# Performance work log

Measured on AMD Instinct MI355X. Metric: run time of the kernel, lower is better.

The kernel has to match this reference:

```python
import jax, jax.numpy as jnp
import numpy as np

D = 1024
SCALE = 10.0  # forward does qk.div(1/10) == qk * 10


def setup_inputs() -> dict:
    key = jax.random.key(0)
    ks = jax.random.split(key, 9)
    B, S = 8, 2048
    lim = 1.0 / np.sqrt(D)  # torch Linear default init range
    return {
        "query": jax.random.normal(ks[0], (B, S, D), jnp.float32),
        "key": jax.random.normal(ks[1], (B, S, D), jnp.float32),
        "value": jax.random.normal(ks[2], (B, S, D), jnp.float32),
        "Wq": jax.random.uniform(ks[3], (D, D), jnp.float32, -lim, lim),
        "bq": jax.random.uniform(ks[4], (D,), jnp.float32, -lim, lim),
        "Wk": jax.random.uniform(ks[5], (D, D), jnp.float32, -lim, lim),
        "bk": jax.random.uniform(ks[6], (D,), jnp.float32, -lim, lim),
        "Wv": jax.random.uniform(ks[7], (D, D), jnp.float32, -lim, lim),
        "bv": jax.random.uniform(ks[8], (D,), jnp.float32, -lim, lim),
    }


def reference(query, key, value, Wq, bq, Wk, bk, Wv, bv):
    # torch Linear: x @ W.T + b
    q = jnp.einsum("bsd,ed->bse", query, Wq) + bq
    k = jnp.einsum("bsd,ed->bse", key, Wk) + bk
    v = jnp.einsum("bsd,ed->bse", value, Wv) + bv
    qk = jnp.einsum("bqd,bkd->bqk", q, k)
    scaled_qk = qk * SCALE  # qk.div(1.0 / scale_factor)
    softmax_qk = jax.nn.softmax(scaled_qk, axis=-1)
    # dropout in eval mode == identity (deterministic reference)
    output = jnp.einsum("bqk,bkd->bqd", softmax_qk, v)
    return (output, softmax_qk)
```

## Files before the change

### kernel.cpp

```cpp
#include <hip/hip_runtime.h>

typedef unsigned short u16;
typedef unsigned int u32;
typedef __bf16 bf16x8 __attribute__((ext_vector_type(8)));
typedef float f32x4 __attribute__((ext_vector_type(4)));

__device__ __forceinline__ u16 bf16_rne(float f) {
  u32 u = __float_as_uint(f);
  u += 0x7fffu + ((u >> 16) & 1u);
  return (u16)(u >> 16);
}
__device__ __forceinline__ float bf16_to_f(u16 h) {
  return __uint_as_float(((u32)h) << 16);
}
__device__ __forceinline__ void gload16(const u16* g, u16* l) {
  __builtin_amdgcn_global_load_lds(
      (const __attribute__((address_space(1))) void*)g,
      (__attribute__((address_space(3))) void*)l, 16, 0, 0);
}

__global__ __launch_bounds__(256) void split_kernel(const float* __restrict__ x,
                                                    u16* __restrict__ hi,
                                                    u16* __restrict__ lo, int n8) {
  int i = blockIdx.x * 256 + threadIdx.x;
  if (i >= n8) return;
  float4 a = ((const float4*)x)[2 * i];
  float4 b = ((const float4*)x)[2 * i + 1];
  float v[8] = {a.x, a.y, a.z, a.w, b.x, b.y, b.z, b.w};
  union { u16 u[8]; uint4 q; } H, L;
#pragma unroll
  for (int j = 0; j < 8; ++j) H.u[j] = bf16_rne(v[j]);
  ((uint4*)hi)[i] = H.q;
  if (lo != nullptr) {
#pragma unroll
    for (int j = 0; j < 8; ++j) L.u[j] = bf16_rne(v[j] - bf16_to_f(H.u[j]));
    ((uint4*)lo)[i] = L.q;
  }
}

__global__ __launch_bounds__(256) void transpose_split(const float* __restrict__ in,
                                                       u16* __restrict__ hiT,
                                                       u16* __restrict__ loT) {
  __shared__ float tile[32][33];
  const int t = threadIdx.x;
  const int r0 = blockIdx.y * 32, c0 = blockIdx.x * 32;
  const int x = t & 31, y = t >> 5;
#pragma unroll
  for (int i = 0; i < 4; ++i)
    tile[y + i * 8][x] = in[(size_t)(r0 + y + i * 8) * 1024 + c0 + x];
  __syncthreads();
#pragma unroll
  for (int i = 0; i < 4; ++i) {
    float v = tile[x][y + i * 8];
    u16 h = bf16_rne(v);
    u16 l = bf16_rne(v - bf16_to_f(h));
    size_t o = (size_t)(c0 + y + i * 8) * 1024 + r0 + x;
    hiT[o] = h;
    loT[o] = l;
  }
}

__global__ __launch_bounds__(256) void zero_vec(float* __restrict__ h) {
  h[blockIdx.x * 256 + threadIdx.x] = 0.f;
}

__global__ __launch_bounds__(256) void colvec_kernel(const float* __restrict__ W,
                                                     const float* __restrict__ b,
                                                     float* __restrict__ h) {
  __shared__ float sb[16];
  const int t = threadIdx.x;
  const int e0 = blockIdx.x * 16;
  if (t < 16) sb[t] = b[e0 + t];
  __syncthreads();
  float a0 = 0.f, a1 = 0.f, a2 = 0.f, a3 = 0.f;
#pragma unroll
  for (int i = 0; i < 16; ++i) {
    const float* row = W + (size_t)(e0 + i) * 1024;
    const float be = sb[i];
    a0 += row[t] * be;
    a1 += row[t + 256] * be;
    a2 += row[t + 512] * be;
    a3 += row[t + 768] * be;
  }
  atomicAdd(&h[t], a0);
  atomicAdd(&h[t + 256], a1);
  atomicAdd(&h[t + 512], a2);
  atomicAdd(&h[t + 768], a3);
}

__global__ __launch_bounds__(256) void rowdot_kernel(const float* __restrict__ X,
                                                     const float* __restrict__ h,
                                                     float* __restrict__ w) {
  const int t = threadIdx.x, lane = t & 63, wv = t >> 6;
  const size_t row = (size_t)blockIdx.x * 4 + wv;
  const float4* xr = (const float4*)(X + row * 1024);
  const float4* hr = (const float4*)h;
  float acc = 0.f;
#pragma unroll
  for (int j = 0; j < 4; ++j) {
    float4 a = xr[lane + j * 64];
    float4 b = hr[lane + j * 64];
    acc += a.x * b.x + a.y * b.y + a.z * b.z + a.w * b.w;
  }
#pragma unroll
  for (int o = 32; o > 0; o >>= 1) acc += __shfl_xor(acc, o, 64);
  if (lane == 0) w[row] = acc;
}

template <int NPROD, int EPI>
__global__ __launch_bounds__(256) void gemm_bt(
    const u16* __restrict__ Ah, const u16* __restrict__ Al,
    const u16* __restrict__ Bh, const u16* __restrict__ Bl,
    const float* __restrict__ bias,
    u16* __restrict__ Ch, u16* __restrict__ Cl,
    float* __restrict__ Cf, float scale, int K,
    int lda, int ldb, int ldc,
    long long batchA, long long batchB, long long batchC) {
  __shared__ u16 sAh[4096];
  __shared__ u16 sBh[4096];
  __shared__ u16 sAl[NPROD == 3 ? 4096 : 64];
  __shared__ u16 sBl[NPROD == 3 ? 4096 : 64];

  const int t = threadIdx.x;
  const int w = t >> 6;
  const int lane = t & 63;
  const int m0 = blockIdx.y * 128;
  const int n0 = blockIdx.x * 128;
  const long long z = blockIdx.z;

  Ah += z * batchA;
  Bh += z * batchB;

  const int rS = t >> 2;
  const int cS = (((t & 3) ^ ((t >> 3) & 3))) * 8;
  const u16* pAh = Ah + (size_t)(m0 + rS) * lda + cS;
  const u16* pBh = Bh + (size_t)(n0 + rS) * ldb + cS;
  const u16* pAl = nullptr;
  const u16* pBl = nullptr;
  if constexpr (NPROD == 3) {
    pAl = Al + z * batchA + (size_t)(m0 + rS) * lda + cS;
    pBl = Bl + z * batchB + (size_t)(n0 + rS) * ldb + cS;
  }

  const int wr = (w >> 1) * 64;
  const int wc = (w & 1) * 64;
  const int fr = lane & 15;
  const int cc = lane >> 4;
  const int fk = (cc ^ ((fr >> 1) & 3)) * 8;

  f32x4 acc[4][4];
#pragma unroll
  for (int i = 0; i < 4; ++i)
#pragma unroll
    for (int j = 0; j < 4; ++j) acc[i][j] = (f32x4){0.f, 0.f, 0.f, 0.f};

  for (int k0 = 0; k0 < K; k0 += 32) {
    __syncthreads();
#pragma unroll
    for (int j = 0; j < 2; ++j) {
      gload16(pAh + (size_t)j * 64 * lda + k0, &sAh[j * 2048 + w * 512]);
      gload16(pBh + (size_t)j * 64 * ldb + k0, &sBh[j * 2048 + w * 512]);
      if constexpr (NPROD == 3) {
        gload16(pAl + (size_t)j * 64 * lda + k0, &sAl[j * 2048 + w * 512]);
        gload16(pBl + (size_t)j * 64 * ldb + k0, &sBl[j * 2048 + w * 512]);
      }
    }
    __syncthreads();
    bf16x8 ah[4], bh[4], al[4], bl[4];
#pragma unroll
    for (int i = 0; i < 4; ++i) {
      ah[i] = *(const bf16x8*)&sAh[(wr + i * 16 + fr) * 32 + fk];
      bh[i] = *(const bf16x8*)&sBh[(wc + i * 16 + fr) * 32 + fk];
      if constexpr (NPROD == 3) {
        al[i] = *(const bf16x8*)&sAl[(wr + i * 16 + fr) * 32 + fk];
        bl[i] = *(const bf16x8*)&sBl[(wc + i * 16 + fr) * 32 + fk];
      }
    }
#pragma unroll
    for (int i = 0; i < 4; ++i)
#pragma unroll
      for (int j = 0; j < 4; ++j) {
        acc[i][j] = __builtin_amdgcn_mfma_f32_16x16x32_bf16(ah[i], bh[j], acc[i][j], 0, 0, 0);
        if constexpr (NPROD == 3) {
          acc[i][j] = __builtin_amdgcn_mfma_f32_16x16x32_bf16(ah[i], bl[j], acc[i][j], 0, 0, 0);
          acc[i][j] = __builtin_amdgcn_mfma_f32_16x16x32_bf16(al[i], bh[j], acc[i][j], 0, 0, 0);
        }
      }
  }

  if constexpr (EPI >= 2) Cf += z * batchC;

#pragma unroll
  for (int i = 0; i < 4; ++i) {
    const int row0 = m0 + wr + i * 16 + ((lane >> 4) << 2);
#pragma unroll
    for (int j = 0; j < 4; ++j) {
      const int col = n0 + wc + j * 16 + (lane & 15);
      if constexpr (EPI == 0) {
        const float b = bias ? bias[col] : 0.0f;
#pragma unroll
        for (int r = 0; r < 4; ++r) {
          float c = acc[i][j][r] + b;
          u16 h = bf16_rne(c);
          u16 l = bf16_rne(c - bf16_to_f(h));
          size_t o = (size_t)(row0 + r) * ldc + col;
          Ch[o] = h;
          Cl[o] = l;
        }
      } else if constexpr (EPI == 1) {
        const float b = bias[col];
        ushort4 pk;
        pk.x = bf16_rne(acc[i][j][0] + b);
        pk.y = bf16_rne(acc[i][j][1] + b);
        pk.z = bf16_rne(acc[i][j][2] + b);
        pk.w = bf16_rne(acc[i][j][3] + b);
        const int bb = row0 >> 11;
        const int s = row0 & 2047;
        *(ushort4*)&Ch[(size_t)bb * 2097152 + (size_t)col * 2048 + s] = pk;
      } else if constexpr (EPI == 2) {
#pragma unroll
        for (int r = 0; r < 4; ++r)
          Cf[(size_t)(row0 + r) * ldc + col] = acc[i][j][r] * scale;
      } else {
        const float wv = bias[(size_t)z * 2048 + col];
#pragma unroll
        for (int r = 0; r < 4; ++r)
          Cf[(size_t)(row0 + r) * ldc + col] = (acc[i][j][r] + wv) * scale;
      }
    }
  }
}

template <int NPROD, int EPI>
__global__ __launch_bounds__(512) void gemm256(
    const u16* __restrict__ Ah, const u16* __restrict__ Al,
    const u16* __restrict__ Bh, const u16* __restrict__ Bl,
    const float* __restrict__ bias,
    u16* __restrict__ Ch, u16* __restrict__ Cl,
    float* __restrict__ Cf, float scale, int K,
    int lda, int ldb, int ldc,
    long long batchA, long long batchB, long long batchC) {
  __shared__ u16 sAh[2][8192];
  __shared__ u16 sBh[2][8192];
  __shared__ u16 sAl[NPROD == 3 ? 16384 : 8];
  __shared__ u16 sBl[NPROD == 3 ? 16384 : 8];

  const int t = threadIdx.x;
  const int w = t >> 6;
  const int lane = t & 63;
  const int m0 = blockIdx.y * 256;
  const int n0 = blockIdx.x * 256;
  const long long z = blockIdx.z;

  const int rS = t >> 2;
  const int cS = ((t & 3) ^ ((rS >> 1) & 3)) * 8;
  const u16* pAh = Ah + z * batchA + (size_t)(m0 + rS) * lda + cS;
  const u16* pBh = Bh + z * batchB + (size_t)(n0 + rS) * ldb + cS;
  const u16* pAl = nullptr;
  const u16* pBl = nullptr;
  if constexpr (NPROD == 3) {
    pAl = Al + z * batchA + (size_t)(m0 + rS) * lda + cS;
    pBl = Bl + z * batchB + (size_t)(n0 + rS) * ldb + cS;
  }

  const int wr = (w >> 2) * 128;
  const int wc = (w & 3) * 64;
  const int fr = lane & 15;
  const int fk = (((lane >> 4) ^ ((fr >> 1) & 3)) * 8);

  f32x4 acc[8][4];
#pragma unroll
  for (int i = 0; i < 8; ++i)
#pragma unroll
    for (int j = 0; j < 4; ++j) acc[i][j] = (f32x4){0.f, 0.f, 0.f, 0.f};

  auto SAH = [&](int b, int k0) {
    gload16(pAh + k0, &sAh[b][w * 512]);
    gload16(pAh + (size_t)128 * lda + k0, &sAh[b][4096 + w * 512]);
  };
  auto SBH = [&](int b, int k0) {
    gload16(pBh + k0, &sBh[b][w * 512]);
    gload16(pBh + (size_t)128 * ldb + k0, &sBh[b][4096 + w * 512]);
  };
  auto SAL = [&](int b, int k0) {
    gload16(pAl + k0, &sAl[b * 8192 + w * 512]);
    gload16(pAl + (size_t)128 * lda + k0, &sAl[b * 8192 + 4096 + w * 512]);
  };
  auto SBL = [&](int b, int k0) {
    gload16(pBl + k0, &sBl[b * 8192 + w * 512]);
    gload16(pBl + (size_t)128 * ldb + k0, &sBl[b * 8192 + 4096 + w * 512]);
  };

  SAH(0, 0);
  SBH(0, 0);
  if constexpr (NPROD == 3) {
    SAL(0, 0);
    SBL(0, 0);
  }
  asm volatile("s_waitcnt vmcnt(0)" ::: "memory");
  __builtin_amdgcn_s_barrier();

  const int nt = K >> 5;
  for (int kt = 0; kt < nt; ++kt) {
    const int cur = kt & 1;
    const int nxt = cur ^ 1;
    const bool pf = (kt + 1) < nt;
    const int kn = (kt + 1) << 5;

    if constexpr (NPROD == 3) {
      bf16x8 bh[4], bl[4];
#pragma unroll
      for (int q = 0; q < 4; ++q) {
        if (q == 0) {
#pragma unroll
          for (int n = 0; n < 4; ++n) {
            bh[n] = *(const bf16x8*)&sBh[cur][(wc + n * 16 + fr) * 32 + fk];
            bl[n] = *(const bf16x8*)&sBl[cur * 8192 + (wc + n * 16 + fr) * 32 + fk];
          }
        }
        bf16x8 a0h = *(const bf16x8*)&sAh[cur][(wr + (2 * q) * 16 + fr) * 32 + fk];
        bf16x8 a1h = *(const bf16x8*)&sAh[cur][(wr + (2 * q + 1) * 16 + fr) * 32 + fk];
        bf16x8 a0l = *(const bf16x8*)&sAl[cur * 8192 + (wr + (2 * q) * 16 + fr) * 32 + fk];
        bf16x8 a1l = *(const bf16x8*)&sAl[cur * 8192 + (wr + (2 * q + 1) * 16 + fr) * 32 + fk];
        if (pf) {
          if (q == 0) { SAH(nxt, kn); SBH(nxt, kn); }
          if (q == 1) { SAL(nxt, kn); SBL(nxt, kn); }
        }
        __builtin_amdgcn_sched_barrier(0);
        __builtin_amdgcn_s_barrier();
        asm volatile("s_waitcnt lgkmcnt(0)" ::: "memory");
        __builtin_amdgcn_sched_barrier(0);
        __builtin_amdgcn_s_setprio(1);
#pragma unroll
        for (int n = 0; n < 4; ++n) {
          acc[2 * q][n] = __builtin_amdgcn_mfma_f32_16x16x32_bf16(a0h, bh[n], acc[2 * q][n], 0, 0, 0);
          acc[2 * q + 1][n] = __builtin_amdgcn_mfma_f32_16x16x32_bf16(a1h, bh[n], acc[2 * q + 1][n], 0, 0, 0);
        }
#pragma unroll
        for (int n = 0; n < 4; ++n) {
          acc[2 * q][n] = __builtin_amdgcn_mfma_f32_16x16x32_bf16(a0h, bl[n], acc[2 * q][n], 0, 0, 0);
          acc[2 * q + 1][n] = __builtin_amdgcn_mfma_f32_16x16x32_bf16(a1h, bl[n], acc[2 * q + 1][n], 0, 0, 0);
        }
#pragma unroll
        for (int n = 0; n < 4; ++n) {
          acc[2 * q][n] = __builtin_amdgcn_mfma_f32_16x16x32_bf16(a0l, bh[n], acc[2 * q][n], 0, 0, 0);
          acc[2 * q + 1][n] = __builtin_amdgcn_mfma_f32_16x16x32_bf16(a1l, bh[n], acc[2 * q + 1][n], 0, 0, 0);
        }
        __builtin_amdgcn_s_setprio(0);
        __builtin_amdgcn_sched_barrier(0);
        if (q == 3) {
          asm volatile("s_waitcnt vmcnt(0)" ::: "memory");
          __builtin_amdgcn_sched_barrier(0);
        }
        __builtin_amdgcn_s_barrier();
      }
    } else {
      bf16x8 bh[4];
#pragma unroll
      for (int q = 0; q < 2; ++q) {
        if (q == 0) {
#pragma unroll
          for (int n = 0; n < 4; ++n)
            bh[n] = *(const bf16x8*)&sBh[cur][(wc + n * 16 + fr) * 32 + fk];
        }
        bf16x8 af[4];
#pragma unroll
        for (int i = 0; i < 4; ++i)
          af[i] = *(const bf16x8*)&sAh[cur][(wr + (4 * q + i) * 16 + fr) * 32 + fk];
        if (pf) {
          if (q == 0) SAH(nxt, kn);
          if (q == 1) SBH(nxt, kn);
        }
        __builtin_amdgcn_sched_barrier(0);
        __builtin_amdgcn_s_barrier();
        asm volatile("s_waitcnt lgkmcnt(0)" ::: "memory");
        __builtin_amdgcn_sched_barrier(0);
        __builtin_amdgcn_s_setprio(1);
#pragma unroll
        for (int i = 0; i < 4; ++i)
#pragma unroll
          for (int n = 0; n < 4; ++n)
            acc[4 * q + i][n] = __builtin_amdgcn_mfma_f32_16x16x32_bf16(af[i], bh[n], acc[4 * q + i][n], 0, 0, 0);
        __builtin_amdgcn_s_setprio(0);
        __builtin_amdgcn_sched_barrier(0);
        if (q == 1) {
          asm volatile("s_waitcnt vmcnt(0)" ::: "memory");
          __builtin_amdgcn_sched_barrier(0);
        }
        __builtin_amdgcn_s_barrier();
      }
    }
  }

  if constexpr (EPI >= 2) Cf += z * batchC;

#pragma unroll
  for (int i = 0; i < 8; ++i) {
    const int row0 = m0 + wr + i * 16 + ((lane >> 4) << 2);
#pragma unroll
    for (int j = 0; j < 4; ++j) {
      const int col = n0 + wc + j * 16 + (lane & 15);
      if constexpr (EPI == 0) {
        const float bsv = bias ? bias[col] : 0.0f;
#pragma unroll
        for (int r = 0; r < 4; ++r) {
          float c = acc[i][j][r] + bsv;
          u16 h = bf16_rne(c);
          u16 l = bf16_rne(c - bf16_to_f(h));
          size_t o = (size_t)(row0 + r) * ldc + col;
          Ch[o] = h;
          Cl[o] = l;
        }
      } else if constexpr (EPI == 1) {
        const float bsv = bias[col];
        ushort4 pk;
        pk.x = bf16_rne(acc[i][j][0] + bsv);
        pk.y = bf16_rne(acc[i][j][1] + bsv);
        pk.z = bf16_rne(acc[i][j][2] + bsv);
        pk.w = bf16_rne(acc[i][j][3] + bsv);
        const int bb = row0 >> 11;
        const int s = row0 & 2047;
        *(ushort4*)&Ch[(size_t)bb * 2097152 + (size_t)col * 2048 + s] = pk;
      } else if constexpr (EPI == 2) {
#pragma unroll
        for (int r = 0; r < 4; ++r)
          Cf[(size_t)(row0 + r) * ldc + col] = acc[i][j][r] * scale;
      } else {
        const float wv = bias[(size_t)z * 2048 + col];
#pragma unroll
        for (int r = 0; r < 4; ++r)
          Cf[(size_t)(row0 + r) * ldc + col] = (acc[i][j][r] + wv) * scale;
      }
    }
  }
}

__global__ __launch_bounds__(256) void softmax_kernel(float* __restrict__ L,
                                                      u16* __restrict__ P) {
  const size_t row = blockIdx.x;
  float* r = L + row * 2048;
  u16* p = P + row * 2048;
  const int t = threadIdx.x;
  const int w = t >> 6;
  const int lane = t & 63;

  float4 v0 = ((const float4*)r)[2 * t];
  float4 v1 = ((const float4*)r)[2 * t + 1];
  float e[8] = {v0.x, v0.y, v0.z, v0.w, v1.x, v1.y, v1.z, v1.w};

  float vm = e[0];
#pragma unroll
  for (int j = 1; j < 8; ++j) vm = fmaxf(vm, e[j]);
#pragma unroll
  for (int o = 32; o > 0; o >>= 1) vm = fmaxf(vm, __shfl_xor(vm, o, 64));
  __shared__ float redm[4], reds[4];
  if (lane == 0) redm[w] = vm;
  __syncthreads();
  vm = fmaxf(fmaxf(redm[0], redm[1]), fmaxf(redm[2], redm[3]));

  float s = 0.f;
#pragma unroll
  for (int j = 0; j < 8; ++j) {
    e[j] = __expf(e[j] - vm);
    s += e[j];
  }
#pragma unroll
  for (int o = 32; o > 0; o >>= 1) s += __shfl_xor(s, o, 64);
  if (lane == 0) reds[w] = s;
  __syncthreads();
  s = reds[0] + reds[1] + reds[2] + reds[3];
  const float inv = 1.0f / s;

  float4 o0, o1;
  o0.x = e[0] * inv; o0.y = e[1] * inv; o0.z = e[2] * inv; o0.w = e[3] * inv;
  o1.x = e[4] * inv; o1.y = e[5] * inv; o1.z = e[6] * inv; o1.w = e[7] * inv;
  ((float4*)r)[2 * t] = o0;
  ((float4*)r)[2 * t + 1] = o1;
  union { u16 u[8]; uint4 q; } pk;
  pk.u[0] = bf16_rne(o0.x); pk.u[1] = bf16_rne(o0.y);
  pk.u[2] = bf16_rne(o0.z); pk.u[3] = bf16_rne(o0.w);
  pk.u[4] = bf16_rne(o1.x); pk.u[5] = bf16_rne(o1.y);
  pk.u[6] = bf16_rne(o1.z); pk.u[7] = bf16_rne(o1.w);
  ((uint4*)p)[t] = pk.q;
}

extern "C" void kernel_launch(void* const* d_in, const int* in_sizes, int n_in,
                              void* d_out, int out_size, void* d_ws, size_t ws_size,
                              hipStream_t stream) {
  const float* Xq = (const float*)d_in[0];
  const float* Xk = (const float*)d_in[1];
  const float* Xv = (const float*)d_in[2];
  const float* Wq = (const float*)d_in[3];
  const float* bq = (const float*)d_in[4];
  const float* Wk = (const float*)d_in[5];
  const float* bk = (const float*)d_in[6];
  const float* Wv = (const float*)d_in[7];
  const float* bv = (const float*)d_in[8];
  (void)bk;

  char* out = (char*)d_out;
  char* ws = (char*)d_ws;

  u16* T_hi = (u16*)(out + 0);
  u16* T_lo = (u16*)(out + 33554432);
  u16* Xq_hi = (u16*)(out + 67108864);
  u16* Xq_lo = (u16*)(out + 100663296);
  u16* Xv_hi = (u16*)(out + 134217728);
  u16* Mt_hi = (u16*)(out + 167772160);
  u16* Mt_lo = (u16*)(out + 171966464);
  float* logits = (float*)(out + 67108864);
  float* outO = (float*)(out + 0);

  u16* WqT_hi = (u16*)(ws + 0);
  u16* WqT_lo = (u16*)(ws + 2097152);
  u16* WkT_hi = (u16*)(ws + 4194304);
  u16* WkT_lo = (u16*)(ws + 6291456);
  u16* Wv_hi = (u16*)(ws + 8388608);
  u16* P = (u16*)(ws + 0);
  float* hvec = (float*)(ws + 67108864);
  float* wvec = (float*)(ws + 67112960);
  u16* Xk_hi = (u16*)(ws + 67178496);
  u16* Xk_lo = (u16*)(ws + 100732928);
  u16* Vt = (u16*)(ws + 134287360);

  transpose_split<<<dim3(32, 32), 256, 0, stream>>>(Wq, WqT_hi, WqT_lo);
  transpose_split<<<dim3(32, 32), 256, 0, stream>>>(Wk, WkT_hi, WkT_lo);
  zero_vec<<<4, 256, 0, stream>>>(hvec);
  colvec_kernel<<<64, 256, 0, stream>>>(Wk, bq, hvec);
  split_kernel<<<512, 256, 0, stream>>>(Wv, Wv_hi, nullptr, 131072);

  split_kernel<<<8192, 256, 0, stream>>>(Xk, Xk_hi, Xk_lo, 2097152);
  rowdot_kernel<<<4096, 256, 0, stream>>>(Xk, hvec, wvec);
  split_kernel<<<8192, 256, 0, stream>>>(Xq, Xq_hi, Xq_lo, 2097152);
  split_kernel<<<8192, 256, 0, stream>>>(Xv, Xv_hi, nullptr, 2097152);

  gemm_bt<3, 0><<<dim3(8, 8, 1), 256, 0, stream>>>(
      WkT_hi, WkT_lo, WqT_hi, WqT_lo, nullptr, Mt_hi, Mt_lo, nullptr, 1.f,
      1024, 1024, 1024, 1024, 0, 0, 0);
  gemm256<1, 1><<<dim3(4, 64, 1), 512, 0, stream>>>(
      Xv_hi, nullptr, Wv_hi, nullptr, bv, Vt, nullptr, nullptr, 1.f,
      1024, 1024, 1024, 1024, 0, 0, 0);
  gemm256<3, 0><<<dim3(4, 64, 1), 512, 0, stream>>>(
      Xq_hi, Xq_lo, Mt_hi, Mt_lo, nullptr, T_hi, T_lo, nullptr, 1.f,
      1024, 1024, 1024, 1024, 0, 0, 0);
  gemm256<3, 3><<<dim3(8, 8, 8), 512, 0, stream>>>(
      T_hi, T_lo, Xk_hi, Xk_lo, wvec, nullptr, nullptr, logits, 10.f,
      1024, 1024, 1024, 2048, 2048LL * 1024, 2048LL * 1024, 2048LL * 2048);
  softmax_kernel<<<16384, 256, 0, stream>>>(logits, P);
  gemm256<1, 2><<<dim3(4, 8, 8), 512, 0, stream>>>(
      P, nullptr, Vt, nullptr, nullptr, nullptr, nullptr, outO, 1.f,
      2048, 2048, 2048, 1024, 2048LL * 2048, 1024LL * 2048, 2048LL * 1024);
}
```

Before: 909.4 us.

## Remix GEMM block order across XCDs and cut per-subtile barriers to one per k-step

```diff
diff --git a/kernel.cpp b/kernel.cpp
--- a/kernel.cpp
+++ b/kernel.cpp
@@ -248,9 +248,19 @@
   const int t = threadIdx.x;
   const int w = t >> 6;
   const int lane = t & 63;
-  const int m0 = blockIdx.y * 256;
-  const int n0 = blockIdx.x * 256;
-  const long long z = blockIdx.z;
+
+  const u32 gx = gridDim.x;
+  const u32 gxy = gridDim.x * gridDim.y;
+  const u32 total = gxy * gridDim.z;
+  const u32 h = blockIdx.x + gridDim.x * (blockIdx.y + gridDim.y * blockIdx.z);
+  const u32 l = (h & 7) * (total >> 3) + (h >> 3);
+  const u32 bz = l / gxy;
+  const u32 rem = l - bz * gxy;
+  const u32 by = rem / gx;
+  const u32 bx = rem - by * gx;
+  const int m0 = by * 256;
+  const int n0 = bx * 256;
+  const long long z = bz;
 
   const int rS = t >> 2;
   const int cS = ((t & 3) ^ ((rS >> 1) & 3)) * 8;
@@ -298,38 +308,36 @@
     SBL(0, 0);
   }
   asm volatile("s_waitcnt vmcnt(0)" ::: "memory");
-  __builtin_amdgcn_s_barrier();
+  asm volatile("s_barrier" ::: "memory");
 
   const int nt = K >> 5;
   for (int kt = 0; kt < nt; ++kt) {
     const int cur = kt & 1;
     const int nxt = cur ^ 1;
-    const bool pf = (kt + 1) < nt;
-    const int kn = (kt + 1) << 5;
+
+    if (kt + 1 < nt) {
+      const int kn = (kt + 1) << 5;
+      SAH(nxt, kn);
+      SBH(nxt, kn);
+      if constexpr (NPROD == 3) {
+        SAL(nxt, kn);
+        SBL(nxt, kn);
+      }
+    }
 
     if constexpr (NPROD == 3) {
       bf16x8 bh[4], bl[4];
 #pragma unroll
+      for (int n = 0; n < 4; ++n) {
+        bh[n] = *(const bf16x8*)&sBh[cur][(wc + n * 16 + fr) * 32 + fk];
+        bl[n] = *(const bf16x8*)&sBl[cur * 8192 + (wc + n * 16 + fr) * 32 + fk];
+      }
+#pragma unroll
       for (int q = 0; q < 4; ++q) {
-        if (q == 0) {
-#pragma unroll
-          for (int n = 0; n < 4; ++n) {
-            bh[n] = *(const bf16x8*)&sBh[cur][(wc + n * 16 + fr) * 32 + fk];
-            bl[n] = *(const bf16x8*)&sBl[cur * 8192 + (wc + n * 16 + fr) * 32 + fk];
-          }
-        }
         bf16x8 a0h = *(const bf16x8*)&sAh[cur][(wr + (2 * q) * 16 + fr) * 32 + fk];
         bf16x8 a1h = *(const bf16x8*)&sAh[cur][(wr + (2 * q + 1) * 16 + fr) * 32 + fk];
         bf16x8 a0l = *(const bf16x8*)&sAl[cur * 8192 + (wr + (2 * q) * 16 + fr) * 32 + fk];
         bf16x8 a1l = *(const bf16x8*)&sAl[cur * 8192 + (wr + (2 * q + 1) * 16 + fr) * 32 + fk];
-        if (pf) {
-          if (q == 0) { SAH(nxt, kn); SBH(nxt, kn); }
-          if (q == 1) { SAL(nxt, kn); SBL(nxt, kn); }
-        }
-        __builtin_amdgcn_sched_barrier(0);
-        __builtin_amdgcn_s_barrier();
-        asm volatile("s_waitcnt lgkmcnt(0)" ::: "memory");
-        __builtin_amdgcn_sched_barrier(0);
         __builtin_amdgcn_s_setprio(1);
 #pragma unroll
         for (int n = 0; n < 4; ++n) {
@@ -347,34 +355,18 @@
           acc[2 * q + 1][n] = __builtin_amdgcn_mfma_f32_16x16x32_bf16(a1l, bh[n], acc[2 * q + 1][n], 0, 0, 0);
         }
         __builtin_amdgcn_s_setprio(0);
-        __builtin_amdgcn_sched_barrier(0);
-        if (q == 3) {
-          asm volatile("s_waitcnt vmcnt(0)" ::: "memory");
-          __builtin_amdgcn_sched_barrier(0);
-        }
-        __builtin_amdgcn_s_barrier();
       }
     } else {
       bf16x8 bh[4];
 #pragma unroll
+      for (int n = 0; n < 4; ++n)
+        bh[n] = *(const bf16x8*)&sBh[cur][(wc + n * 16 + fr) * 32 + fk];
+#pragma unroll
       for (int q = 0; q < 2; ++q) {
-        if (q == 0) {
-#pragma unroll
-          for (int n = 0; n < 4; ++n)
-            bh[n] = *(const bf16x8*)&sBh[cur][(wc + n * 16 + fr) * 32 + fk];
-        }
         bf16x8 af[4];
 #pragma unroll
         for (int i = 0; i < 4; ++i)
           af[i] = *(const bf16x8*)&sAh[cur][(wr + (4 * q + i) * 16 + fr) * 32 + fk];
-        if (pf) {
-          if (q == 0) SAH(nxt, kn);
-          if (q == 1) SBH(nxt, kn);
-        }
-        __builtin_amdgcn_sched_barrier(0);
-        __builtin_amdgcn_s_barrier();
-        asm volatile("s_waitcnt lgkmcnt(0)" ::: "memory");
-        __builtin_amdgcn_sched_barrier(0);
         __builtin_amdgcn_s_setprio(1);
 #pragma unroll
         for (int i = 0; i < 4; ++i)
@@ -382,14 +374,11 @@
           for (int n = 0; n < 4; ++n)
             acc[4 * q + i][n] = __builtin_amdgcn_mfma_f32_16x16x32_bf16(af[i], bh[n], acc[4 * q + i][n], 0, 0, 0);
         __builtin_amdgcn_s_setprio(0);
-        __builtin_amdgcn_sched_barrier(0);
-        if (q == 1) {
-          asm volatile("s_waitcnt vmcnt(0)" ::: "memory");
-          __builtin_amdgcn_sched_barrier(0);
-        }
-        __builtin_amdgcn_s_barrier();
       }
     }
+
+    asm volatile("s_waitcnt vmcnt(0)" ::: "memory");
+    asm volatile("s_barrier" ::: "memory");
   }
 
   if constexpr (EPI >= 2) Cf += z * batchC;
```

New measurement: 911.8 us. Within noise of the previous version (+0.3%).
